# Performance work log

Hardware: AMD Instinct MI355X
Metric: run time of the kernel (lower is better)

Reference implementation:

```python
import math
import jax, jax.numpy as jnp
import numpy as np

B, CIN, COUT, K, S = 2, 64, 64, 3, 18  # batch, channels, kernel size per dim, spatial size per dim


def setup_inputs() -> dict:
    key = jax.random.key(0)
    k1, k2 = jax.random.split(key)
    inputs = jax.random.normal(k1, (B, CIN, S, S, S, S), dtype=jnp.float32)
    std = 1.0 / math.sqrt(CIN * K ** 4)  # matches init_weight: 1/sqrt(in_channels * n_offsets)
    kernel = jax.random.uniform(k2, (K ** 4, CIN, COUT), dtype=jnp.float32, minval=-std, maxval=std)
    return {"inputs": inputs, "kernel": kernel}


def reference(inputs, kernel):
    # kernel: [k0*k1*k2*k3, Cin, Cout], offsets enumerated row-major over the 4 kernel dims.
    # Equivalent to the per-offset matmul + shift-accumulate in conv4d (valid padding,
    # stride=1, dilation=1), expressed as a single 4-spatial-dim XLA convolution.
    cin, cout = kernel.shape[1], kernel.shape[2]
    w = kernel.reshape(K, K, K, K, cin, cout).transpose(5, 4, 0, 1, 2, 3)  # OIWXYZ
    out = jax.lax.conv_general_dilated(
        inputs, w,
        window_strides=(1, 1, 1, 1),
        padding='VALID',
        rhs_dilation=(1, 1, 1, 1),
        dimension_numbers=('NCWXYZ', 'OIWXYZ', 'NCWXYZ'),
    )  # [B, Cout, 16, 16, 16, 16]
    return out
```

## Files before the change

### kernel.cpp

```cpp
#include <hip/hip_runtime.h>


typedef __attribute__((ext_vector_type(8))) short bf16x8;
typedef __attribute__((ext_vector_type(4))) float f32x4;
typedef __attribute__((ext_vector_type(8))) unsigned short ushort8;
typedef unsigned short u16;
typedef unsigned int u32;

#define S_OFF_BYTES 663552u
#define WS_NEEDED   27537408u

__device__ __forceinline__ u16 f2bf(float f) {
    u32 u = __float_as_uint(f);
    u += 0x7FFFu + ((u >> 16) & 1u);
    return (u16)(u >> 16);
}

__global__ __launch_bounds__(256) void wprep(const float* __restrict__ ker, u16* __restrict__ wg) {
    const int g = blockIdx.x * 256 + threadIdx.x;
    const int l = g & 63, ks = (g >> 6) & 1, rt = (g >> 7) & 3, off = g >> 9;
    const int co  = rt * 16 + (l & 15);
    const int ci0 = ks * 32 + (l >> 4) * 8;
    const float* p = ker + (size_t)off * 4096 + co;
    ushort8 v;
#pragma unroll
    for (int e = 0; e < 8; ++e) v[e] = f2bf(p[(size_t)(ci0 + e) * 64]);
    *(ushort8*)(wg + (size_t)g * 8) = v;
}

__global__ __launch_bounds__(256) void sprep(const float* __restrict__ in, u16* __restrict__ s) {
    __shared__ u16 L[64 * 330];
    const int blk = blockIdx.x;
    const int b = blk / 324, wx = blk - b * 324;
    const float* src = in + (size_t)b * 6718464 + (wx / 18) * 5832 + (wx % 18) * 324;
    const int t = threadIdx.x;
    for (int i = t; i < 5184; i += 256) {
        const int ci = i / 81, j = i - ci * 81;
        float4 v = *(const float4*)(src + (size_t)ci * 104976 + j * 4);
        u32* q = (u32*)&L[ci * 330 + j * 4];
        q[0] = f2bf(v.x) | ((u32)f2bf(v.y) << 16);
        q[1] = f2bf(v.z) | ((u32)f2bf(v.w) << 16);
    }
    __syncthreads();
    u16* dst = s + (size_t)blk * 20736;
    for (int i = t; i < 2592; i += 256) {
        const int ks = i / 1296, r4 = i - ks * 1296;
        const int rem = r4 >> 2, g = r4 & 3;
        ushort8 v;
#pragma unroll
        for (int e = 0; e < 8; ++e) v[e] = L[(ks * 32 + g * 8 + e) * 330 + rem];
        const int gp = g ^ ((rem >> 1) & 3);
        *(ushort8*)(dst + ks * 10368 + rem * 32 + gp * 8) = v;
    }
}

__global__ __launch_bounds__(256, 2)
void conv4d_main(const u16* __restrict__ wg, const u16* __restrict__ s, float* __restrict__ out) {
    __shared__ u16 A[3][6144];
    __shared__ u16 Bq[2][10368];

    const int bid = blockIdx.x;
    const int bs  = (bid & 7) * 64 + (bid >> 3);
    const int b   = bs >> 8;
    const int w   = (bs >> 4) & 15;
    const int x   = bs & 15;

    const int t  = threadIdx.x, wv = t >> 6, l = t & 63;
    const int lg = l >> 4, ll = l & 15;

    f32x4 acc[4][4];
#pragma unroll
    for (int i = 0; i < 4; ++i)
#pragma unroll
        for (int j = 0; j < 4; ++j) acc[i][j] = (f32x4){0.f, 0.f, 0.f, 0.f};

    const u16* sb = s + (size_t)(b * 324 + w * 18 + x) * 20736;

#define STAGE_A(p2, kz2, slot)                                                           \
    do {                                                                                 \
        const int kwx_ = (p2) >> 1, ks2_ = (p2) & 1;                                     \
        _Pragma("unroll")                                                                \
        for (int c_ = 0; c_ < 3; ++c_) {                                                 \
            const u16* src_ = wg + (size_t)(kwx_ * 9 + c_ * 3 + (kz2)) * 4096            \
                              + wv * 1024 + ks2_ * 512 + l * 8;                          \
            __builtin_amdgcn_global_load_lds(                                            \
                (const __attribute__((address_space(1))) u32*)src_,                      \
                (__attribute__((address_space(3))) u32*)&A[slot][c_ * 2048 + wv * 512 + l * 8], \
                16, 0, 0);                                                               \
        }                                                                                \
    } while (0)

#define STAGE_B(h)                                                                       \
    do {                                                                                 \
        const int kwx_ = (h) >> 1, ks_ = (h) & 1;                                        \
        const int kw_ = kwx_ / 3, kx_ = kwx_ - kw_ * 3;                                  \
        const u16* src_ = sb + (size_t)(kw_ * 18 + kx_) * 20736 + ks_ * 10368;           \
        const int base_ = wv * 324;                                                      \
        _Pragma("unroll")                                                                \
        for (int k_ = 0; k_ < 5; ++k_) {                                                 \
            const int i_ = base_ + k_ * 64 + l;                                          \
            __builtin_amdgcn_global_load_lds(                                            \
                (const __attribute__((address_space(1))) u32*)(src_ + (size_t)i_ * 8),   \
                (__attribute__((address_space(3))) u32*)&Bq[(h) & 1][i_ * 8], 16, 0, 0); \
        }                                                                                \
        if (l < 4) {                                                                     \
            const int i_ = base_ + 320 + l;                                              \
            __builtin_amdgcn_global_load_lds(                                            \
                (const __attribute__((address_space(1))) u32*)(src_ + (size_t)i_ * 8),   \
                (__attribute__((address_space(3))) u32*)&Bq[(h) & 1][i_ * 8], 16, 0, 0); \
        }                                                                                \
    } while (0)

#define PHASE_COMPUTE(qc, Tb)                                                            \
    do {                                                                                 \
        bf16x8 af[3][4];                                                                 \
        bf16x8 bb[6];                                                                    \
        _Pragma("unroll")                                                                \
        for (int ky_ = 0; ky_ < 3; ++ky_)                                                \
            _Pragma("unroll")                                                            \
            for (int rt_ = 0; rt_ < 4; ++rt_)                                            \
                af[ky_][rt_] = *(const bf16x8*)&A[qc][ky_ * 2048 + rt_ * 512 + l * 8];   \
        _Pragma("unroll")                                                                \
        for (int q_ = 0; q_ < 6; ++q_) {                                                 \
            const int rem_ = (4 * wv + q_) * 18 + ll + (qc);                             \
            bb[q_] = *(const bf16x8*)&(Tb)[rem_ * 32 + ((lg ^ ((rem_ >> 1) & 3)) << 3)]; \
        }                                                                                \
        __builtin_amdgcn_s_setprio(1);                                                   \
        _Pragma("unroll")                                                                \
        for (int ky_ = 0; ky_ < 3; ++ky_)                                                \
            _Pragma("unroll")                                                            \
            for (int ct_ = 0; ct_ < 4; ++ct_)                                            \
                _Pragma("unroll")                                                        \
                for (int rt_ = 0; rt_ < 4; ++rt_)                                        \
                    acc[rt_][ct_] = __builtin_amdgcn_mfma_f32_16x16x32_bf16(             \
                        af[ky_][rt_], bb[ct_ + ky_], acc[rt_][ct_], 0, 0, 0);            \
        __builtin_amdgcn_s_setprio(0);                                                   \
    } while (0)

#define WAITBAR(N)                                                                       \
    do {                                                                                 \
        asm volatile("s_waitcnt vmcnt(" #N ")" ::: "memory");                            \
        __builtin_amdgcn_sched_barrier(0);                                               \
        __builtin_amdgcn_s_barrier();                                                    \
    } while (0)

    STAGE_A(0, 0, 0);
    STAGE_A(0, 1, 1);
    STAGE_B(0);
    WAITBAR(0);

    for (int p = 0; p < 18; ++p) {
        const u16* Tb = Bq[p & 1];

        STAGE_A(p, 2, 2);
        PHASE_COMPUTE(0, Tb);
        WAITBAR(3);

        if (p < 17) {
            STAGE_A(p + 1, 0, 0);
            STAGE_B(p + 1);
        }
        PHASE_COMPUTE(1, Tb);
        if (p < 17) WAITBAR(9);
        else        WAITBAR(0);

        if (p < 17) STAGE_A(p + 1, 1, 1);
        PHASE_COMPUTE(2, Tb);
        if (p < 17) WAITBAR(3);
    }
#undef STAGE_A
#undef STAGE_B
#undef PHASE_COMPUTE
#undef WAITBAR

    float* ob = out + (size_t)b * 4194304 + (size_t)w * 4096 + (size_t)x * 256;
#pragma unroll
    for (int rt = 0; rt < 4; ++rt) {
        const int co0 = rt * 16 + 4 * lg;
#pragma unroll
        for (int ct = 0; ct < 4; ++ct) {
            const int base = (4 * wv + ct) * 16 + ll;
#pragma unroll
            for (int r = 0; r < 4; ++r)
                ob[(size_t)(co0 + r) * 65536 + base] = acc[rt][ct][r];
        }
    }
}

__global__ __launch_bounds__(512, 2)
void conv4d_mfma(const float* __restrict__ in, const float* __restrict__ ker,
                 float* __restrict__ out) {
    __shared__ unsigned short T[18 * 18 * 64];
    __shared__ unsigned short Wt[2][64 * 64];
    const int bx = blockIdx.x;
    const int b = bx >> 8, wsp = (bx >> 4) & 15, x = bx & 15;
    const int t = threadIdx.x, wv = t >> 6, l = t & 63;
    const int lg = l >> 4, ll = l & 15;
    const float* inb = in + (size_t)b * 6718464 + wsp * 5832 + x * 324;
    f32x4 acc[4][2];
#pragma unroll
    for (int i = 0; i < 4; ++i)
#pragma unroll
        for (int j = 0; j < 2; ++j) acc[i][j] = (f32x4){0.f, 0.f, 0.f, 0.f};
#pragma unroll
    for (int f0 = 0; f0 < 4096; f0 += 512) {
        const int f = f0 + t, ci = f >> 6, co = f & 63;
        Wt[0][co * 64 + ((((ci >> 3) ^ (co & 7)) << 3) | (ci & 7))] = f2bf(ker[f]);
    }
    for (int off = 0; off < 81; ++off) {
        const int sub = off % 9;
        if (sub == 0) {
            const int kw = off / 27, kx = (off / 9) % 3;
            const float* p = inb + kw * 5832 + kx * 324;
            for (int f = t; f < 18 * 18 * 64; f += 512) {
                const int ci = f / 324, rem = f - ci * 324, zp = rem % 18;
                T[rem * 64 + ((((ci >> 3) ^ (zp & 7)) << 3) | (ci & 7))] =
                    f2bf(p[(size_t)ci * 104976 + rem]);
            }
        }
        if (off + 1 < 81) {
            const float* p = ker + (off + 1) * 4096;
            unsigned short* wb = Wt[(off + 1) & 1];
#pragma unroll
            for (int f0 = 0; f0 < 4096; f0 += 512) {
                const int f = f0 + t, ci = f >> 6, co = f & 63;
                wb[co * 64 + ((((ci >> 3) ^ (co & 7)) << 3) | (ci & 7))] = f2bf(p[f]);
            }
        }
        if (sub == 0) __syncthreads();
        const int ky = sub / 3, kz = sub - ky * 3;
        const int zp = ll + kz, zs = zp & 7;
#pragma unroll
        for (int ks = 0; ks < 2; ++ks) {
            bf16x8 af[4];
#pragma unroll
            for (int rt = 0; rt < 4; ++rt)
                af[rt] = *(const bf16x8*)&Wt[off & 1][(rt * 16 + ll) * 64 + (((lg + 4 * ks) ^ (ll & 7)) << 3)];
#pragma unroll
            for (int ct = 0; ct < 2; ++ct) {
                const int rem = (2 * wv + ct + ky) * 18 + zp;
                const bf16x8 bfr = *(const bf16x8*)&T[rem * 64 + (((lg + 4 * ks) ^ zs) << 3)];
#pragma unroll
                for (int rt = 0; rt < 4; ++rt)
                    acc[rt][ct] = __builtin_amdgcn_mfma_f32_16x16x32_bf16(af[rt], bfr, acc[rt][ct], 0, 0, 0);
            }
        }
        __syncthreads();
    }
    float* ob = out + (size_t)b * 4194304 + wsp * 4096 + x * 256;
#pragma unroll
    for (int rt = 0; rt < 4; ++rt) {
        const int co0 = rt * 16 + 4 * lg;
#pragma unroll
        for (int ct = 0; ct < 2; ++ct) {
            const int base = (2 * wv + ct) * 16 + ll;
#pragma unroll
            for (int r = 0; r < 4; ++r)
                ob[(size_t)(co0 + r) * 65536 + base] = acc[rt][ct][r];
        }
    }
}

extern "C" void kernel_launch(void* const* d_in, const int* in_sizes, int n_in,
                              void* d_out, int out_size, void* d_ws, size_t ws_size,
                              hipStream_t stream) {
    const float* in  = (const float*)d_in[0];
    const float* ker = (const float*)d_in[1];
    float* out = (float*)d_out;
    if (ws_size >= (size_t)WS_NEEDED) {
        u16* wg = (u16*)d_ws;
        u16* s  = (u16*)((char*)d_ws + S_OFF_BYTES);
        wprep<<<dim3(162), dim3(256), 0, stream>>>(ker, wg);
        sprep<<<dim3(648), dim3(256), 0, stream>>>(in, s);
        conv4d_main<<<dim3(512), dim3(256), 0, stream>>>(wg, s, out);
    } else {
        conv4d_mfma<<<dim3(512), dim3(512), 0, stream>>>(in, ker, out);
    }
}
```

Baseline: 93.26 us.

## Double-buffer LDS fragment reads in registers across MFMA phases

Reworks the main loop into a flat sequence of 54 phases, unrolled by 6. Each phase first issues the global-to-LDS staging for the A slice two phases ahead, then loads the next phase's A and B fragments from LDS into a second register bank, then runs the current phase's MFMAs. The goal is to hide LDS read latency behind matrix compute instead of stalling on it at the start of each phase. The cost is that the A/B fragment registers are doubled, which raises VGPR pressure and risks spills or lower occupancy. Each phase also now waits for all outstanding global loads (vmcnt(0)) rather than allowing partial counts, which gives less slack to hide memory latency.

```diff
diff --git a/kernel.cpp b/kernel.cpp
--- a/kernel.cpp
+++ b/kernel.cpp
@@ -76,16 +76,19 @@
 
     const u16* sb = s + (size_t)(b * 324 + w * 18 + x) * 20736;
 
-#define STAGE_A(p2, kz2, slot)                                                           \
-    do {                                                                                 \
-        const int kwx_ = (p2) >> 1, ks2_ = (p2) & 1;                                     \
+    bf16x8 af[2][3][4];
+    bf16x8 bb[2][6];
+
+#define STAGE_A(tk, KZ)                                                                  \
+    do {                                                                                 \
+        const int kwx_ = (tk) >> 1, ks2_ = (tk) & 1;                                     \
         _Pragma("unroll")                                                                \
         for (int c_ = 0; c_ < 3; ++c_) {                                                 \
-            const u16* src_ = wg + (size_t)(kwx_ * 9 + c_ * 3 + (kz2)) * 4096            \
+            const u16* src_ = wg + (size_t)(kwx_ * 9 + c_ * 3 + (KZ)) * 4096             \
                               + wv * 1024 + ks2_ * 512 + l * 8;                          \
             __builtin_amdgcn_global_load_lds(                                            \
                 (const __attribute__((address_space(1))) u32*)src_,                      \
-                (__attribute__((address_space(3))) u32*)&A[slot][c_ * 2048 + wv * 512 + l * 8], \
+                (__attribute__((address_space(3))) u32*)&A[KZ][c_ * 2048 + wv * 512 + l * 8], \
                 16, 0, 0);                                                               \
         }                                                                                \
     } while (0)
@@ -111,20 +114,24 @@
         }                                                                                \
     } while (0)
 
-#define PHASE_COMPUTE(qc, Tb)                                                            \
-    do {                                                                                 \
-        bf16x8 af[3][4];                                                                 \
-        bf16x8 bb[6];                                                                    \
+#define READ_REGS(BK, UP, QQ)                                                            \
+    do {                                                                                 \
+        const int tk_ = (UP) / 3;                                                        \
+        const u16* Tb_ = Bq[tk_ & 1];                                                    \
         _Pragma("unroll")                                                                \
         for (int ky_ = 0; ky_ < 3; ++ky_)                                                \
             _Pragma("unroll")                                                            \
             for (int rt_ = 0; rt_ < 4; ++rt_)                                            \
-                af[ky_][rt_] = *(const bf16x8*)&A[qc][ky_ * 2048 + rt_ * 512 + l * 8];   \
-        _Pragma("unroll")                                                                \
-        for (int q_ = 0; q_ < 6; ++q_) {                                                 \
-            const int rem_ = (4 * wv + q_) * 18 + ll + (qc);                             \
-            bb[q_] = *(const bf16x8*)&(Tb)[rem_ * 32 + ((lg ^ ((rem_ >> 1) & 3)) << 3)]; \
-        }                                                                                \
+                af[BK][ky_][rt_] = *(const bf16x8*)&A[QQ][ky_ * 2048 + rt_ * 512 + l * 8]; \
+        _Pragma("unroll")                                                                \
+        for (int j_ = 0; j_ < 6; ++j_) {                                                 \
+            const int rem_ = (4 * wv + j_) * 18 + ll + (QQ);                             \
+            bb[BK][j_] = *(const bf16x8*)&Tb_[rem_ * 32 + ((lg ^ ((rem_ >> 1) & 3)) << 3)]; \
+        }                                                                                \
+    } while (0)
+
+#define MFMA_PHASE(BK)                                                                   \
+    do {                                                                                 \
         __builtin_amdgcn_s_setprio(1);                                                   \
         _Pragma("unroll")                                                                \
         for (int ky_ = 0; ky_ < 3; ++ky_)                                                \
@@ -133,45 +140,41 @@
                 _Pragma("unroll")                                                        \
                 for (int rt_ = 0; rt_ < 4; ++rt_)                                        \
                     acc[rt_][ct_] = __builtin_amdgcn_mfma_f32_16x16x32_bf16(             \
-                        af[ky_][rt_], bb[ct_ + ky_], acc[rt_][ct_], 0, 0, 0);            \
+                        af[BK][ky_][rt_], bb[BK][ct_ + ky_], acc[rt_][ct_], 0, 0, 0);    \
         __builtin_amdgcn_s_setprio(0);                                                   \
     } while (0)
 
-#define WAITBAR(N)                                                                       \
-    do {                                                                                 \
-        asm volatile("s_waitcnt vmcnt(" #N ")" ::: "memory");                            \
-        __builtin_amdgcn_sched_barrier(0);                                               \
-        __builtin_amdgcn_s_barrier();                                                    \
-    } while (0)
-
-    STAGE_A(0, 0, 0);
-    STAGE_A(0, 1, 1);
+    STAGE_A(0, 0);
+    STAGE_A(0, 1);
     STAGE_B(0);
-    WAITBAR(0);
-
-    for (int p = 0; p < 18; ++p) {
-        const u16* Tb = Bq[p & 1];
-
-        STAGE_A(p, 2, 2);
-        PHASE_COMPUTE(0, Tb);
-        WAITBAR(3);
-
-        if (p < 17) {
-            STAGE_A(p + 1, 0, 0);
-            STAGE_B(p + 1);
-        }
-        PHASE_COMPUTE(1, Tb);
-        if (p < 17) WAITBAR(9);
-        else        WAITBAR(0);
-
-        if (p < 17) STAGE_A(p + 1, 1, 1);
-        PHASE_COMPUTE(2, Tb);
-        if (p < 17) WAITBAR(3);
+    asm volatile("s_waitcnt vmcnt(0)" ::: "memory");
+    __builtin_amdgcn_sched_barrier(0);
+    __builtin_amdgcn_s_barrier();
+    READ_REGS(0, 0, 0);
+
+    for (int u6 = 0; u6 < 54; u6 += 6) {
+#pragma unroll
+        for (int m = 0; m < 6; ++m) {
+            const int u = u6 + m;
+            if (u < 52) STAGE_A((u + 2) / 3, ((m + 2) % 3));
+            if ((m % 3) == 1) {
+                const int p_ = u / 3;
+                if (p_ < 17) STAGE_B(p_ + 1);
+            }
+            if (u < 53) READ_REGS(((m + 1) & 1), (u + 1), ((m + 1) % 3));
+            __builtin_amdgcn_sched_barrier(0);
+            MFMA_PHASE((m & 1));
+            if (u < 53) {
+                asm volatile("s_waitcnt vmcnt(0)" ::: "memory");
+                __builtin_amdgcn_sched_barrier(0);
+                __builtin_amdgcn_s_barrier();
+            }
+        }
     }
 #undef STAGE_A
 #undef STAGE_B
-#undef PHASE_COMPUTE
-#undef WAITBAR
+#undef READ_REGS
+#undef MFMA_PHASE
 
     float* ob = out + (size_t)b * 4194304 + (size_t)w * 4096 + (size_t)x * 256;
 #pragma unroll
```

Result: no change. 93.53 us (+0.3%).
